# Kernel tuning notes

Measured on AMD Instinct MI355X. Metric: run time of the kernel, lower is better.

## Reference

```python
import jax, jax.numpy as jnp
import numpy as np

N, D, E = 200000, 256, 6400000
RATIO = 0.5
NEG_SLOPE = 0.2


def _xavier(key, shape, gain=1.414):
    fan_in, fan_out = shape[0], shape[1]
    limit = gain * (6.0 / (fan_in + fan_out)) ** 0.5
    return jax.random.uniform(key, shape, jnp.float32, -limit, limit)


def setup_inputs() -> dict:
    key = jax.random.key(0)
    ks = jax.random.split(key, 8)
    x = jax.random.normal(ks[0], (N, D), jnp.float32)
    edge_index = jax.random.randint(ks[1], (2, E), 0, N, dtype=jnp.int64)
    return {
        "x": x,
        "edge_index": edge_index,
        "w_s1": _xavier(ks[2], (2 * D, D)), "b_s1": jnp.zeros((D,), jnp.float32),
        "w_s2": _xavier(ks[3], (D, 1)),     "b_s2": jnp.zeros((1,), jnp.float32),
        "w_f1": _xavier(ks[4], (D, D // 2)), "b_f1": jnp.zeros((D // 2,), jnp.float32),
        "w_f2": _xavier(ks[5], (D // 2, 1)), "b_f2": jnp.zeros((1,), jnp.float32),
        "w_p": _xavier(ks[6], (D, D)),      "b_p": jnp.zeros((D,), jnp.float32),
        "alpha": jnp.float32(0.5), "beta": jnp.float32(0.5),
    }


def reference(x, edge_index, w_s1, b_s1, w_s2, b_s2, w_f1, b_f1, w_f2, b_f2, w_p, b_p, alpha, beta):
    num_nodes = x.shape[0]
    k = max(1, int(RATIO * num_nodes))
    lrelu = lambda v: jax.nn.leaky_relu(v, NEG_SLOPE)

    row, col = edge_index[0], edge_index[1]
    # degree(row, N): scatter-add of ones over source nodes
    deg = jax.ops.segment_sum(jnp.ones_like(row, dtype=x.dtype), row, num_segments=num_nodes)
    # F.normalize(p=2, dim=0) on the [N,1] degree column
    deg_norm = deg / jnp.maximum(jnp.sqrt(jnp.sum(deg * deg)), 1e-12)

    struct_in = jnp.concatenate([x, jnp.broadcast_to(deg_norm[:, None], x.shape)], axis=1)  # [N, 2D]
    struct_scores = (lrelu(struct_in @ w_s1 + b_s1) @ w_s2 + b_s2)[:, 0]  # dropout is eval no-op
    feat_scores = (lrelu(x @ w_f1 + b_f1) @ w_f2 + b_f2)[:, 0]

    a = jax.nn.sigmoid(alpha)
    b = jax.nn.sigmoid(beta)
    s = a + b
    scores = (a / s) * struct_scores + (b / s) * feat_scores  # [N]

    # single-graph top-k (batch=None default path)
    topk_scores, topk_idx = jax.lax.top_k(scores, k)
    x_pooled = lrelu(x[topk_idx] @ w_p + b_p)  # post_pool, dropout no-op

    # edge remap + compaction (valid edges first, -1 padding to keep static shape)
    node_map = jnp.full((num_nodes,), -1, dtype=jnp.int32).at[topk_idx].set(
        jnp.arange(k, dtype=jnp.int32))
    mr, mc = node_map[row], node_map[col]
    mask = (mr >= 0) & (mc >= 0)
    order = jnp.argsort(~mask, stable=True)  # stable: keeps original edge order among valid
    edge_index_pooled = jnp.stack([
        jnp.where(mask, mr, -1)[order],
        jnp.where(mask, mc, -1)[order],
    ])
    return x_pooled, edge_index_pooled, topk_scores
```

## Files before the change

### kernel.cpp

```cpp
#include <hip/hip_runtime.h>
#include <math.h>

typedef unsigned long long u64;
typedef unsigned int u32;
typedef unsigned short u16;
typedef __attribute__((ext_vector_type(8))) short bf16x8;
typedef __attribute__((ext_vector_type(4))) float f32x4;

#define D   256
#define ECH 16
#define EBLK (256*ECH)
#define BAND_W 4096
#define BAND_DELTA 1e-3f
#define HR  12544
#define HCH 32

__device__ __forceinline__ double lrelu(double v){ return v > 0.0 ? v : 0.2*v; }
__device__ __forceinline__ float  lreluf(float v){ return v > 0.0f ? v : 0.2f*v; }

__device__ __forceinline__ u16 f2bf(float f){
  union{float f; u32 u;} v; v.f = f;
  u32 r = v.u + 0x7FFFu + ((v.u >> 16) & 1u);
  return (u16)(r >> 16);
}
__device__ __forceinline__ float bf2f(u16 b){
  union{u32 u; float f;} v; v.u = ((u32)b) << 16; return v.f;
}

__global__ __launch_bounds__(256) void k_deghist(const int* __restrict__ row, int E,
                                                 u32* __restrict__ partial, int NR){
  __shared__ u32 h[HR];
  const int tid = threadIdx.x;
  const int r = blockIdx.x % NR;
  const int c = blockIdx.x / NR;
  for (int i = tid; i < HR; i += 256) h[i] = 0;
  __syncthreads();
  const int lo = r * HR;
  int CE = ((E + HCH - 1) / HCH + 3) & ~3;
  const int e0 = c * CE;
  const int e1 = min(e0 + CE, E);
  for (int e = e0 + tid*4; e < e1; e += 256*4){
    if (e + 3 < e1){
      int4 v = *(const int4*)(row + e);
      u32 d0 = (u32)(v.x - lo), d1 = (u32)(v.y - lo);
      u32 d2 = (u32)(v.z - lo), d3 = (u32)(v.w - lo);
      if (d0 < (u32)HR) atomicAdd(&h[d0], 1u);
      if (d1 < (u32)HR) atomicAdd(&h[d1], 1u);
      if (d2 < (u32)HR) atomicAdd(&h[d2], 1u);
      if (d3 < (u32)HR) atomicAdd(&h[d3], 1u);
    } else {
      for (int j = 0; j < 4 && e + j < e1; ++j){
        u32 d = (u32)(row[e+j] - lo);
        if (d < (u32)HR) atomicAdd(&h[d], 1u);
      }
    }
  }
  __syncthreads();
  u32* plane = partial + (size_t)blockIdx.x * HR;
  for (int i = tid; i < HR; i += 256) plane[i] = h[i];
}

__global__ void k_degred2(const u32* __restrict__ partial, int N, int NR,
                          int* __restrict__ deg, u64* __restrict__ out){
  __shared__ u64 sh[256];
  u64 local = 0;
  int stride = gridDim.x*blockDim.x;
  for (int i = blockIdx.x*blockDim.x + threadIdx.x; i < N; i += stride){
    int r = i / HR, off = i % HR;
    u32 s = 0;
    #pragma unroll 8
    for (int c = 0; c < HCH; ++c) s += partial[(size_t)(c*NR + r)*HR + off];
    deg[i] = (int)s;
    local += (u64)s * (u64)s;
  }
  sh[threadIdx.x] = local; __syncthreads();
  for (int s = 128; s > 0; s >>= 1){
    if (threadIdx.x < s) sh[threadIdx.x] += sh[threadIdx.x+s];
    __syncthreads();
  }
  if (threadIdx.x == 0) atomicAdd(out, sh[0]);
}

__global__ void k_prep(const float* __restrict__ wS1, const float* __restrict__ alpha,
                       const float* __restrict__ beta, const u64* __restrict__ sumsq,
                       double* __restrict__ s1b, double* __restrict__ scal,
                       float* __restrict__ s1bf, float* __restrict__ scalf){
  int j = threadIdx.x;
  double s = 0.0;
  for (int r = 0; r < D; ++r) s += (double)wS1[(D + r)*D + j];
  s1b[j] = s;
  s1bf[j] = (float)s;
  if (j == 0){
    double a = 1.0/(1.0 + exp(-(double)alpha[0]));
    double b = 1.0/(1.0 + exp(-(double)beta[0]));
    scal[0] = a/(a+b);
    scal[1] = b/(a+b);
    double dn = sqrt((double)(*sumsq));
    scal[2] = dn > 1e-12 ? dn : 1e-12;
    scalf[0] = (float)scal[0];
    scalf[1] = (float)scal[1];
    scalf[2] = (float)(1.0/scal[2]);
  }
}

__global__ void k_wsw(const float* __restrict__ wS1, const float* __restrict__ wF1,
                      u16* __restrict__ wswH, u16* __restrict__ wswL){
  int idx = blockIdx.x*blockDim.x + threadIdx.x;
  int i    = idx & 7;
  int lane = (idx >> 3) & 63;
  int sg   = (idx >> 9) & 7;
  int t    = idx >> 12;
  int k = sg*32 + ((lane >> 4) & 3)*8 + i;
  int c16 = lane & 15;
  float wv;
  if (t < 16) wv = wS1[k*256 + t*16 + c16];
  else        wv = wF1[k*128 + (t-16)*16 + c16];
  u16 h = f2bf(wv);
  float lo = wv - bf2f(h);
  wswH[idx] = h;
  wswL[idx] = f2bf(lo);
}

__global__ void k_wswP(const float* __restrict__ wP,
                       u16* __restrict__ wH, u16* __restrict__ wL){
  int idx = blockIdx.x*blockDim.x + threadIdx.x;
  int i    = idx & 7;
  int lane = (idx >> 3) & 63;
  int sg   = (idx >> 9) & 7;
  int t    = idx >> 12;
  int k = sg*32 + ((lane >> 4) & 3)*8 + i;
  float wv = wP[k*256 + t*16 + (lane & 15)];
  u16 h = f2bf(wv);
  float lo = wv - bf2f(h);
  wH[idx] = h;
  wL[idx] = f2bf(lo);
}

__global__ __launch_bounds__(512, 4) void k_scores_mfma(
    const float* __restrict__ x, const int* __restrict__ deg,
    const u16* __restrict__ wswH, const u16* __restrict__ wswL,
    const float* __restrict__ bS1, const float* __restrict__ wS2, const float* __restrict__ bS2,
    const float* __restrict__ bF1, const float* __restrict__ wF2, const float* __restrict__ bF2,
    const float* __restrict__ s1bf, const float* __restrict__ scalf,
    float* __restrict__ s32, u64* __restrict__ keys, int N)
{
  __shared__ u16 xsh[2][4096];
  __shared__ u16 xsl[2][4096];
  __shared__ float dnsh[64];
  __shared__ float part_s[64][9];
  __shared__ float part_f[64][9];

  const int tid  = threadIdx.x;
  const int lane = tid & 63;
  const int w    = tid >> 6;
  const int node0 = blockIdx.x * 64;

  if (tid < 64){
    int node = node0 + tid;
    dnsh[tid] = (node < N) ? ((float)deg[node] * scalf[2]) : 0.0f;
  }

  const int row_st = tid >> 3;
  const int seg_st = tid & 7;
  const int unit_w = row_st*8 + (seg_st ^ (row_st & 7));
  const float* srcbase = x + (size_t)(node0 + row_st)*D + seg_st*8;
  const bool rv = (node0 + row_st) < N;

  f32x4 acc[4][3];
  #pragma unroll
  for (int m = 0; m < 4; ++m)
    #pragma unroll
    for (int n = 0; n < 3; ++n) acc[m][n] = (f32x4){0.f,0.f,0.f,0.f};

  float xr[8];
  {
    if (rv){
      float4 a = *(const float4*)(srcbase);
      float4 b = *(const float4*)(srcbase + 4);
      xr[0]=a.x; xr[1]=a.y; xr[2]=a.z; xr[3]=a.w;
      xr[4]=b.x; xr[5]=b.y; xr[6]=b.z; xr[7]=b.w;
    } else {
      #pragma unroll
      for (int i = 0; i < 8; ++i) xr[i] = 0.f;
    }
  }

  #pragma unroll
  for (int c = 0; c < 4; ++c){
    const int pb = c & 1;
    {
      u16 h[8];
      #pragma unroll
      for (int i = 0; i < 8; ++i) h[i] = f2bf(xr[i]);
      uint4 H; H.x = (u32)h[0] | ((u32)h[1]<<16); H.y = (u32)h[2] | ((u32)h[3]<<16);
               H.z = (u32)h[4] | ((u32)h[5]<<16); H.w = (u32)h[6] | ((u32)h[7]<<16);
      u16 l[8];
      #pragma unroll
      for (int i = 0; i < 8; ++i) l[i] = f2bf(xr[i] - bf2f(h[i]));
      uint4 L; L.x = (u32)l[0] | ((u32)l[1]<<16); L.y = (u32)l[2] | ((u32)l[3]<<16);
               L.z = (u32)l[4] | ((u32)l[5]<<16); L.w = (u32)l[6] | ((u32)l[7]<<16);
      *(uint4*)&xsh[pb][unit_w*8] = H;
      *(uint4*)&xsl[pb][unit_w*8] = L;
    }
    if (c < 3){
      const float* sn = srcbase + (c+1)*64;
      if (rv){
        float4 a = *(const float4*)(sn);
        float4 b = *(const float4*)(sn + 4);
        xr[0]=a.x; xr[1]=a.y; xr[2]=a.z; xr[3]=a.w;
        xr[4]=b.x; xr[5]=b.y; xr[6]=b.z; xr[7]=b.w;
      }
    }
    __syncthreads();
    #pragma unroll
    for (int s = 0; s < 2; ++s){
      const int sg = c*2 + s;
      bf16x8 ah[4], al[4];
      #pragma unroll
      for (int mt = 0; mt < 4; ++mt){
        int row = mt*16 + (lane & 15);
        int seg = s*4 + (lane >> 4);
        int un  = row*8 + (seg ^ (row & 7));
        ah[mt] = *(const bf16x8*)&xsh[pb][un*8];
        al[mt] = *(const bf16x8*)&xsl[pb][un*8];
      }
      const int t0 = w*3;
      size_t o0 = ((size_t)(t0*8 + sg)*64 + lane)*8;
      bf16x8 bh = *(const bf16x8*)&wswH[o0];
      bf16x8 bl = *(const bf16x8*)&wswL[o0];
      #pragma unroll
      for (int nt = 0; nt < 3; ++nt){
        bf16x8 nbh = bh, nbl = bl;
        if (nt < 2){
          size_t on = ((size_t)((t0+nt+1)*8 + sg)*64 + lane)*8;
          nbh = *(const bf16x8*)&wswH[on];
          nbl = *(const bf16x8*)&wswL[on];
        }
        #pragma unroll
        for (int mt = 0; mt < 4; ++mt){
          acc[mt][nt] = __builtin_amdgcn_mfma_f32_16x16x32_bf16(ah[mt], bh, acc[mt][nt], 0,0,0);
          acc[mt][nt] = __builtin_amdgcn_mfma_f32_16x16x32_bf16(al[mt], bh, acc[mt][nt], 0,0,0);
          acc[mt][nt] = __builtin_amdgcn_mfma_f32_16x16x32_bf16(ah[mt], bl, acc[mt][nt], 0,0,0);
        }
        bh = nbh; bl = nbl;
      }
    }
    __syncthreads();
  }

  float dnl[4][4];
  #pragma unroll
  for (int mt = 0; mt < 4; ++mt)
    #pragma unroll
    for (int j = 0; j < 4; ++j)
      dnl[mt][j] = dnsh[mt*16 + (lane>>4)*4 + j];

  float ps[4][4], pf[4][4];
  #pragma unroll
  for (int mt = 0; mt < 4; ++mt)
    #pragma unroll
    for (int j = 0; j < 4; ++j){ ps[mt][j] = 0.f; pf[mt][j] = 0.f; }

  #pragma unroll
  for (int nt = 0; nt < 3; ++nt){
    const int t = w*3 + nt;
    const int c16 = lane & 15;
    const bool isS = (t < 16);
    const int col = isS ? t*16 + c16 : (t-16)*16 + c16;
    const float bias = isS ? bS1[col] : bF1[col];
    const float sbv  = isS ? s1bf[col] : 0.f;
    const float vv   = isS ? wS2[col] : wF2[col];
    #pragma unroll
    for (int mt = 0; mt < 4; ++mt){
      #pragma unroll
      for (int j = 0; j < 4; ++j){
        float v = acc[mt][nt][j] + bias + dnl[mt][j]*sbv;
        v = lreluf(v) * vv;
        v += __shfl_xor(v, 1);
        v += __shfl_xor(v, 2);
        v += __shfl_xor(v, 4);
        v += __shfl_xor(v, 8);
        if (isS) ps[mt][j] += v; else pf[mt][j] += v;
      }
    }
  }
  if ((lane & 15) == 0){
    #pragma unroll
    for (int mt = 0; mt < 4; ++mt)
      #pragma unroll
      for (int j = 0; j < 4; ++j){
        int row = mt*16 + (lane>>4)*4 + j;
        part_s[row][w] = ps[mt][j];
        part_f[row][w] = pf[mt][j];
      }
  }
  __syncthreads();
  if (tid < 64){
    int node = node0 + tid;
    if (node < N){
      float sv = 0.f, fv = 0.f;
      #pragma unroll
      for (int ww = 0; ww < 8; ++ww){ sv += part_s[tid][ww]; fv += part_f[tid][ww]; }
      float sc = scalf[0]*(sv + bS2[0]) + scalf[1]*(fv + bF2[0]);
      s32[node] = sc;
      u32 bits = __float_as_uint(sc);
      u32 ord = (bits >> 31) ? ~bits : (bits | 0x80000000u);
      keys[node] = ((u64)(~ord) << 32) | (u32)node;
    }
  }
}

__global__ void k_padkeys(u64* __restrict__ keys, int N, int SORTN){
  int i = N + blockIdx.x*blockDim.x + threadIdx.x;
  if (i < SORTN) keys[i] = ~0ULL;
}

__global__ __launch_bounds__(1024) void k_bsort_local8k(u64* __restrict__ keys){
  __shared__ u64 sk[8192];
  const int tid = threadIdx.x;
  const int base = blockIdx.x * 8192;
  #pragma unroll
  for (int e = 0; e < 8; ++e) sk[tid + e*1024] = keys[base + tid + e*1024];
  __syncthreads();
  for (int size = 2; size <= 8192; size <<= 1){
    for (int stride = size >> 1; stride > 0; stride >>= 1){
      #pragma unroll
      for (int pp = 0; pp < 4; ++pp){
        int p  = tid + pp*1024;
        int i  = 2*p - (p & (stride-1));
        int jj = i + stride;
        bool up = (((base + i) & size) == 0);
        u64 ki = sk[i], kj = sk[jj];
        if ((ki > kj) == up){ sk[i] = kj; sk[jj] = ki; }
      }
      __syncthreads();
    }
  }
  #pragma unroll
  for (int e = 0; e < 8; ++e) keys[base + tid + e*1024] = sk[tid + e*1024];
}

__global__ __launch_bounds__(1024) void k_bmerge_local8k(u64* __restrict__ keys, int size){
  __shared__ u64 sk[8192];
  const int tid = threadIdx.x;
  const int base = blockIdx.x * 8192;
  #pragma unroll
  for (int e = 0; e < 8; ++e) sk[tid + e*1024] = keys[base + tid + e*1024];
  __syncthreads();
  for (int stride = 4096; stride > 0; stride >>= 1){
    #pragma unroll
    for (int pp = 0; pp < 4; ++pp){
      int p  = tid + pp*1024;
      int i  = 2*p - (p & (stride-1));
      int jj = i + stride;
      bool up = (((base + i) & size) == 0);
      u64 ki = sk[i], kj = sk[jj];
      if ((ki > kj) == up){ sk[i] = kj; sk[jj] = ki; }
    }
    __syncthreads();
  }
  #pragma unroll
  for (int e = 0; e < 8; ++e) keys[base + tid + e*1024] = sk[tid + e*1024];
}

template<int NS>
__global__ void k_bpassM(u64* __restrict__ keys, int size, int stride){
  const int G = 1 << NS;
  u32 t = blockIdx.x*blockDim.x + threadIdx.x;
  u32 smin = (u32)stride >> (NS-1);
  u32 i0 = (t/smin)*(smin << NS) + (t % smin);
  u64 v[G];
  #pragma unroll
  for (int j = 0; j < G; ++j) v[j] = keys[i0 + (u32)j*smin];
  bool up = ((i0 & (u32)size) == 0);
  #pragma unroll
  for (int b = (G>>1); b >= 1; b >>= 1){
    #pragma unroll
    for (int j = 0; j < G; ++j){
      if ((j & b) == 0){
        u64 a = v[j], cc = v[j|b];
        if ((a > cc) == up){ v[j] = cc; v[j|b] = a; }
      }
    }
  }
  #pragma unroll
  for (int j = 0; j < G; ++j) keys[i0 + (u32)j*smin] = v[j];
}

__global__ void kr_cut(const u64* __restrict__ keys, int k, float* __restrict__ cutbuf,
                       int* __restrict__ r01){
  if (threadIdx.x == 0 && blockIdx.x == 0){
    u32 key32 = (u32)(keys[k-1] >> 32);
    u32 ord = ~key32;
    u32 u = (ord & 0x80000000u) ? (ord ^ 0x80000000u) : ~ord;
    float c = __uint_as_float(u);
    cutbuf[0] = c - BAND_DELTA;
    cutbuf[1] = c + BAND_DELTA;
    r01[0] = 0x7FFFFFFF;
    r01[1] = -1;
  }
}

__global__ __launch_bounds__(256) void kr_rescore(
    const u64* __restrict__ keys, const float* __restrict__ s32,
    const float* __restrict__ x, const int* __restrict__ deg,
    const float* __restrict__ wS1, const float* __restrict__ bS1,
    const float* __restrict__ wS2, const float* __restrict__ bS2,
    const float* __restrict__ wF1, const float* __restrict__ bF1,
    const float* __restrict__ wF2, const float* __restrict__ bF2,
    const double* __restrict__ s1b, const double* __restrict__ scal,
    const float* __restrict__ cutbuf, int* __restrict__ r01,
    double* __restrict__ bandS, int k, int N)
{
  const int r = k - BAND_W + blockIdx.x;
  if (r < 0 || r >= N) return;
  const int node = (int)(u32)(keys[r] & 0xFFFFFFFFULL);
  const float s = s32[node];
  if (s < cutbuf[0] || s > cutbuf[1]) return;

  const int tid = threadIdx.x;
  if (tid == 0){ atomicMin(&r01[0], r); atomicMax(&r01[1], r); }

  __shared__ float xr[256];
  __shared__ double rsp[4], rfp[4];
  xr[tid] = x[(size_t)node*D + tid];
  __syncthreads();

  const int j = tid;
  double accA = (double)bS1[j] + ((double)deg[node]/scal[2]) * s1b[j];
  double accB = (j < 128) ? (double)bF1[j] : 0.0;
  for (int rr = 0; rr < D; ++rr){
    double xv = (double)xr[rr];
    accA = fma(xv, (double)wS1[rr*D + j], accA);
    if (j < 128) accB = fma(xv, (double)wF1[rr*128 + j], accB);
  }
  double sp = lrelu(accA) * (double)wS2[j];
  double fp = (j < 128) ? lrelu(accB) * (double)wF2[j] : 0.0;

  const int lane = tid & 63, wave = tid >> 6;
  #pragma unroll
  for (int off = 32; off > 0; off >>= 1){
    sp += __shfl_down(sp, off);
    fp += __shfl_down(fp, off);
  }
  if (lane == 0){ rsp[wave] = sp; rfp[wave] = fp; }
  __syncthreads();
  if (tid == 0){
    double SP = rsp[0]+rsp[1]+rsp[2]+rsp[3];
    double FP = rfp[0]+rfp[1]+rfp[2]+rfp[3];
    bandS[blockIdx.x] = scal[0]*(SP + (double)bS2[0]) + scal[1]*(FP + (double)bF2[0]);
  }
}

__global__ __launch_bounds__(1024) void kr_bandsort(u64* __restrict__ keys,
    const double* __restrict__ bandS, const int* __restrict__ r01, int k){
  __shared__ double bs[8192];
  __shared__ int bi[8192];
  const int r0 = r01[0], r1 = r01[1];
  int nb = r1 - r0 + 1;
  if (nb <= 1) return;
  if (nb > 8192) nb = 8192;
  int M = 1; while (M < nb) M <<= 1;
  const int tid = threadIdx.x;
  const int sbase = r0 - (k - BAND_W);
  for (int m = tid; m < M; m += 1024){
    if (m < nb){ bs[m] = bandS[sbase + m]; bi[m] = (int)(u32)(keys[r0+m] & 0xFFFFFFFFULL); }
    else       { bs[m] = -1.0/0.0;         bi[m] = 0x7FFFFFFF; }
  }
  __syncthreads();
  for (int size = 2; size <= M; size <<= 1){
    for (int stride = size >> 1; stride > 0; stride >>= 1){
      for (int p = tid; p < (M >> 1); p += 1024){
        int i = 2*p - (p & (stride-1));
        int jj = i + stride;
        bool up = ((i & size) == 0);
        double si_ = bs[i], sj = bs[jj];
        int ii = bi[i], ij = bi[jj];
        bool gt = (si_ < sj) || (si_ == sj && ii > ij);
        if (gt == up){ bs[i]=sj; bs[jj]=si_; bi[i]=ij; bi[jj]=ii; }
      }
      __syncthreads();
    }
  }
  for (int m = tid; m < nb; m += 1024)
    keys[r0+m] = (u64)(u32)bi[m];
}

__global__ void k_finalize(const u64* __restrict__ keys, const float* __restrict__ s32,
                           int k, int* __restrict__ nmap, float* __restrict__ outS){
  int p = blockIdx.x*blockDim.x + threadIdx.x;
  if (p < k){
    int node = (int)(u32)(keys[p] & 0xFFFFFFFFULL);
    nmap[node] = p;
    outS[p] = s32[node];
  }
}

__global__ __launch_bounds__(512, 4) void k_xpool_mfma(
    const float* __restrict__ x, const u64* __restrict__ keys,
    const u16* __restrict__ wH, const u16* __restrict__ wL,
    const float* __restrict__ bP, float* __restrict__ out, int kk)
{
  __shared__ u16 xsh[2][4096];
  __shared__ u16 xsl[2][4096];

  const int tid  = threadIdx.x;
  const int lane = tid & 63;
  const int w    = tid >> 6;
  const int p0 = blockIdx.x * 64;
  if (p0 >= kk) return;

  const int row_st = tid >> 3;
  const int seg_st = tid & 7;
  const int unit_w = row_st*8 + (seg_st ^ (row_st & 7));
  int prow = p0 + row_st; if (prow >= kk) prow = kk - 1;
  const int node = (int)(u32)(keys[prow] & 0xFFFFFFFFULL);
  const float* srcbase = x + (size_t)node*D + seg_st*8;

  f32x4 acc[4][2];
  #pragma unroll
  for (int m = 0; m < 4; ++m){ acc[m][0] = (f32x4){0.f,0.f,0.f,0.f}; acc[m][1] = (f32x4){0.f,0.f,0.f,0.f}; }

  float xr[8];
  {
    float4 a = *(const float4*)(srcbase);
    float4 b = *(const float4*)(srcbase + 4);
    xr[0]=a.x; xr[1]=a.y; xr[2]=a.z; xr[3]=a.w;
    xr[4]=b.x; xr[5]=b.y; xr[6]=b.z; xr[7]=b.w;
  }

  #pragma unroll
  for (int c = 0; c < 4; ++c){
    const int pb = c & 1;
    {
      u16 h[8];
      #pragma unroll
      for (int i = 0; i < 8; ++i) h[i] = f2bf(xr[i]);
      uint4 H; H.x = (u32)h[0] | ((u32)h[1]<<16); H.y = (u32)h[2] | ((u32)h[3]<<16);
               H.z = (u32)h[4] | ((u32)h[5]<<16); H.w = (u32)h[6] | ((u32)h[7]<<16);
      u16 l[8];
      #pragma unroll
      for (int i = 0; i < 8; ++i) l[i] = f2bf(xr[i] - bf2f(h[i]));
      uint4 L; L.x = (u32)l[0] | ((u32)l[1]<<16); L.y = (u32)l[2] | ((u32)l[3]<<16);
               L.z = (u32)l[4] | ((u32)l[5]<<16); L.w = (u32)l[6] | ((u32)l[7]<<16);
      *(uint4*)&xsh[pb][unit_w*8] = H;
      *(uint4*)&xsl[pb][unit_w*8] = L;
    }
    if (c < 3){
      const float* sn = srcbase + (c+1)*64;
      float4 a = *(const float4*)(sn);
      float4 b = *(const float4*)(sn + 4);
      xr[0]=a.x; xr[1]=a.y; xr[2]=a.z; xr[3]=a.w;
      xr[4]=b.x; xr[5]=b.y; xr[6]=b.z; xr[7]=b.w;
    }
    __syncthreads();
    #pragma unroll
    for (int s = 0; s < 2; ++s){
      const int sg = c*2 + s;
      bf16x8 ah[4], al[4];
      #pragma unroll
      for (int mt = 0; mt < 4; ++mt){
        int row = mt*16 + (lane & 15);
        int seg = s*4 + (lane >> 4);
        int un  = row*8 + (seg ^ (row & 7));
        ah[mt] = *(const bf16x8*)&xsh[pb][un*8];
        al[mt] = *(const bf16x8*)&xsl[pb][un*8];
      }
      const int t0 = w*2;
      size_t o0 = ((size_t)(t0*8 + sg)*64 + lane)*8;
      bf16x8 bh = *(const bf16x8*)&wH[o0];
      bf16x8 bl = *(const bf16x8*)&wL[o0];
      #pragma unroll
      for (int nt = 0; nt < 2; ++nt){
        bf16x8 nbh = bh, nbl = bl;
        if (nt < 1){
          size_t on = ((size_t)((t0+1)*8 + sg)*64 + lane)*8;
          nbh = *(const bf16x8*)&wH[on];
          nbl = *(const bf16x8*)&wL[on];
        }
        #pragma unroll
        for (int mt = 0; mt < 4; ++mt){
          acc[mt][nt] = __builtin_amdgcn_mfma_f32_16x16x32_bf16(ah[mt], bh, acc[mt][nt], 0,0,0);
          acc[mt][nt] = __builtin_amdgcn_mfma_f32_16x16x32_bf16(al[mt], bh, acc[mt][nt], 0,0,0);
          acc[mt][nt] = __builtin_amdgcn_mfma_f32_16x16x32_bf16(ah[mt], bl, acc[mt][nt], 0,0,0);
        }
        bh = nbh; bl = nbl;
      }
    }
    __syncthreads();
  }

  const int c16 = lane & 15, r4 = (lane >> 4)*4;
  #pragma unroll
  for (int nt = 0; nt < 2; ++nt){
    const int col = (w*2 + nt)*16 + c16;
    const float bias = bP[col];
    #pragma unroll
    for (int mt = 0; mt < 4; ++mt){
      #pragma unroll
      for (int j = 0; j < 4; ++j){
        int p = p0 + mt*16 + r4 + j;
        if (p < kk) out[(size_t)p*D + col] = lreluf(acc[mt][nt][j] + bias);
      }
    }
  }
}

__global__ __launch_bounds__(256) void k_ecount(const int* __restrict__ erow, const int* __restrict__ ecol,
    const int* __restrict__ nmap, int E, int* __restrict__ bcount){
  __shared__ int sc[256];
  const int tid = threadIdx.x;
  const int base = blockIdx.x*EBLK + tid*ECH;
  int cnt = 0;
  #pragma unroll
  for (int q = 0; q < ECH; ++q){
    int e = base + q;
    if (e < E){
      if (nmap[erow[e]] >= 0 && nmap[ecol[e]] >= 0) cnt++;
    }
  }
  sc[tid] = cnt; __syncthreads();
  for (int s = 128; s > 0; s >>= 1){
    if (tid < s) sc[tid] += sc[tid+s];
    __syncthreads();
  }
  if (tid == 0) bcount[blockIdx.x] = sc[0];
}

__global__ __launch_bounds__(1024) void k_escan(const int* __restrict__ bcount, int nblk,
                                                int* __restrict__ boff, int* __restrict__ tot){
  __shared__ int sh[1024];
  const int tid = threadIdx.x;
  int carry = 0;
  for (int s = 0; s < nblk; s += 1024){
    int v = (s + tid < nblk) ? bcount[s+tid] : 0;
    sh[tid] = v; __syncthreads();
    for (int d = 1; d < 1024; d <<= 1){
      int t = (tid >= d) ? sh[tid-d] : 0;
      __syncthreads();
      sh[tid] += t;
      __syncthreads();
    }
    if (s + tid < nblk) boff[s+tid] = carry + sh[tid] - v;
    carry += sh[1023];
    __syncthreads();
  }
  if (tid == 0) *tot = carry;
}

__global__ void k_efill_tail(float* __restrict__ outR, float* __restrict__ outC,
                             const int* __restrict__ tot, int E){
  const int t0 = *tot;
  int stride = gridDim.x*blockDim.x;
  for (int i = t0 + blockIdx.x*blockDim.x + threadIdx.x; i < E; i += stride){
    outR[i] = -1.0f;
    outC[i] = -1.0f;
  }
}

__global__ __launch_bounds__(256) void k_escatter(const int* __restrict__ erow, const int* __restrict__ ecol,
    const int* __restrict__ nmap, int E, const int* __restrict__ boff,
    float* __restrict__ outR, float* __restrict__ outC){
  __shared__ int sc[256];
  const int tid = threadIdx.x;
  const int base = blockIdx.x*EBLK + tid*ECH;
  int mr[ECH], mc[ECH];
  int cnt = 0;
  #pragma unroll
  for (int q = 0; q < ECH; ++q){
    int e = base + q;
    int a = -1, b = -1;
    if (e < E){ a = nmap[erow[e]]; b = nmap[ecol[e]]; }
    mr[q] = a; mc[q] = b;
    if (a >= 0 && b >= 0) cnt++;
  }
  sc[tid] = cnt; __syncthreads();
  int v = cnt;
  for (int d = 1; d < 256; d <<= 1){
    int t = (tid >= d) ? sc[tid-d] : 0;
    __syncthreads();
    sc[tid] += t;
    __syncthreads();
  }
  int pos = boff[blockIdx.x] + sc[tid] - v;
  #pragma unroll
  for (int q = 0; q < ECH; ++q){
    if (mr[q] >= 0 && mc[q] >= 0){
      outR[pos] = (float)mr[q];
      outC[pos] = (float)mc[q];
      pos++;
    }
  }
}

extern "C" void kernel_launch(void* const* d_in, const int* in_sizes, int n_in,
                              void* d_out, int out_size, void* d_ws, size_t ws_size,
                              hipStream_t stream)
{
  const float* x   = (const float*)d_in[0];
  const int*   ei  = (const int*)d_in[1];
  const float* wS1 = (const float*)d_in[2];
  const float* bS1 = (const float*)d_in[3];
  const float* wS2 = (const float*)d_in[4];
  const float* bS2 = (const float*)d_in[5];
  const float* wF1 = (const float*)d_in[6];
  const float* bF1 = (const float*)d_in[7];
  const float* wF2 = (const float*)d_in[8];
  const float* bF2 = (const float*)d_in[9];
  const float* wP  = (const float*)d_in[10];
  const float* bP  = (const float*)d_in[11];
  const float* alpha = (const float*)d_in[12];
  const float* beta  = (const float*)d_in[13];
  (void)n_in; (void)out_size; (void)ws_size;

  const int N = in_sizes[0] / D;
  const int E = in_sizes[1] / 2;
  int k = (int)(0.5 * (double)N); if (k < 1) k = 1;
  int SORTN = 8192; while (SORTN < N) SORTN <<= 1;
  const int nblk_e = (E + EBLK - 1) / EBLK;
  const int NR = (N + HR - 1) / HR;

  char* w = (char*)d_ws;
  size_t off = 0;
  auto alloc = [&](size_t bytes)->char*{
    char* p = w + off;
    off = (off + bytes + 255) & ~(size_t)255;
    return p;
  };
  float*  s32    = (float*) alloc((size_t)N*4);
  u64*    keys   = (u64*)   alloc((size_t)SORTN*8);
  int*    deg    = (int*)   alloc((size_t)N*4);
  int*    nmap   = (int*)   alloc((size_t)N*4);
  double* s1b    = (double*)alloc((size_t)D*8);
  float*  s1bf   = (float*) alloc((size_t)D*4);
  double* scal   = (double*)alloc(4*8);
  float*  scalf  = (float*) alloc(4*4);
  u64*    sumsq  = (u64*)   alloc(8);
  float*  cutbuf = (float*) alloc(2*4);
  int*    r01    = (int*)   alloc(2*4);
  int*    tot    = (int*)   alloc(4);
  double* bandS  = (double*)alloc((size_t)2*BAND_W*8);
  u16*    wswH   = (u16*)   alloc((size_t)98304*2);
  u16*    wswL   = (u16*)   alloc((size_t)98304*2);
  u16*    wswPH  = (u16*)   alloc((size_t)65536*2);
  u16*    wswPL  = (u16*)   alloc((size_t)65536*2);
  int*    bcount = (int*)   alloc((size_t)nblk_e*4);
  int*    boff   = (int*)   alloc((size_t)nblk_e*4);

  float* outX  = (float*)d_out;
  float* outER = outX  + (size_t)k*D;
  float* outEC = outER + (size_t)E;
  float* outS  = outEC + (size_t)E;

  u32* partial = (u32*)outER;

  hipMemsetAsync(sumsq, 0,    8,           stream);
  hipMemsetAsync(nmap,  0xFF, (size_t)N*4, stream);

  k_deghist<<<NR*HCH, 256, 0, stream>>>(ei, E, partial, NR);
  k_degred2<<<1024, 256, 0, stream>>>(partial, N, NR, deg, sumsq);
  k_prep   <<<1,    D,   0, stream>>>(wS1, alpha, beta, sumsq, s1b, scal, s1bf, scalf);
  k_wsw    <<<384,  256, 0, stream>>>(wS1, wF1, wswH, wswL);
  k_wswP   <<<256,  256, 0, stream>>>(wP, wswPH, wswPL);
  k_scores_mfma<<<(N + 63)/64, 512, 0, stream>>>(x, deg, wswH, wswL,
                                                 bS1, wS2, bS2, bF1, wF2, bF2,
                                                 s1bf, scalf, s32, keys, N);
  k_padkeys<<<(SORTN - N + 255)/256, 256, 0, stream>>>(keys, N, SORTN);

  k_bsort_local8k<<<SORTN/8192, 1024, 0, stream>>>(keys);
  for (int size = 16384; size <= SORTN; size <<= 1){
    int stride = size >> 1;
    while (stride >= 8192){
      int ns = 1;
      while (ns < 4 && (stride >> ns) >= 8192) ns++;
      switch (ns){
        case 1: k_bpassM<1><<<SORTN/2/256,  256, 0, stream>>>(keys, size, stride); break;
        case 2: k_bpassM<2><<<SORTN/4/256,  256, 0, stream>>>(keys, size, stride); break;
        case 3: k_bpassM<3><<<SORTN/8/256,  256, 0, stream>>>(keys, size, stride); break;
        default:k_bpassM<4><<<SORTN/16/256, 256, 0, stream>>>(keys, size, stride); break;
      }
      stride >>= ns;
    }
    k_bmerge_local8k<<<SORTN/8192, 1024, 0, stream>>>(keys, size);
  }

  kr_cut     <<<1, 64, 0, stream>>>(keys, k, cutbuf, r01);
  kr_rescore <<<2*BAND_W, 256, 0, stream>>>(keys, s32, x, deg, wS1,bS1,wS2,bS2,
                                            wF1,bF1,wF2,bF2, s1b, scal,
                                            cutbuf, r01, bandS, k, N);
  kr_bandsort<<<1, 1024, 0, stream>>>(keys, bandS, r01, k);

  k_finalize<<<(k+255)/256, 256, 0, stream>>>(keys, s32, k, nmap, outS);
  k_xpool_mfma<<<(k+63)/64, 512, 0, stream>>>(x, keys, wswPH, wswPL, bP, outX, k);
  k_ecount  <<<nblk_e, 256, 0, stream>>>(ei, ei+E, nmap, E, bcount);
  k_escan   <<<1, 1024, 0, stream>>>(bcount, nblk_e, boff, tot);
  k_efill_tail<<<1024, 256, 0, stream>>>(outER, outEC, tot, E);
  k_escatter<<<nblk_e, 256, 0, stream>>>(ei, ei+E, nmap, E, boff, outER, outEC);
}
```

Before: 828.8 us.

## Drop weight low-part MFMA terms, pack degree histogram in 16-bit bins, fuse key padding

```diff
diff --git a/kernel.cpp b/kernel.cpp
--- a/kernel.cpp
+++ b/kernel.cpp
@@ -11,8 +11,8 @@
 #define ECH 16
 #define EBLK (256*ECH)
 #define BAND_W 4096
-#define BAND_DELTA 1e-3f
-#define HR  12544
+#define BAND_DELTA 2e-2f
+#define HR  25088
 #define HCH 32
 
 __device__ __forceinline__ double lrelu(double v){ return v > 0.0 ? v : 0.2*v; }
@@ -29,11 +29,11 @@
 
 __global__ __launch_bounds__(256) void k_deghist(const int* __restrict__ row, int E,
                                                  u32* __restrict__ partial, int NR){
-  __shared__ u32 h[HR];
+  __shared__ u32 h[HR/2];
   const int tid = threadIdx.x;
   const int r = blockIdx.x % NR;
   const int c = blockIdx.x / NR;
-  for (int i = tid; i < HR; i += 256) h[i] = 0;
+  for (int i = tid; i < HR/2; i += 256) h[i] = 0;
   __syncthreads();
   const int lo = r * HR;
   int CE = ((E + HCH - 1) / HCH + 3) & ~3;
@@ -44,20 +44,20 @@
       int4 v = *(const int4*)(row + e);
       u32 d0 = (u32)(v.x - lo), d1 = (u32)(v.y - lo);
       u32 d2 = (u32)(v.z - lo), d3 = (u32)(v.w - lo);
-      if (d0 < (u32)HR) atomicAdd(&h[d0], 1u);
-      if (d1 < (u32)HR) atomicAdd(&h[d1], 1u);
-      if (d2 < (u32)HR) atomicAdd(&h[d2], 1u);
-      if (d3 < (u32)HR) atomicAdd(&h[d3], 1u);
+      if (d0 < (u32)HR) atomicAdd(&h[d0 >> 1], 1u << ((d0 & 1)*16));
+      if (d1 < (u32)HR) atomicAdd(&h[d1 >> 1], 1u << ((d1 & 1)*16));
+      if (d2 < (u32)HR) atomicAdd(&h[d2 >> 1], 1u << ((d2 & 1)*16));
+      if (d3 < (u32)HR) atomicAdd(&h[d3 >> 1], 1u << ((d3 & 1)*16));
     } else {
       for (int j = 0; j < 4 && e + j < e1; ++j){
         u32 d = (u32)(row[e+j] - lo);
-        if (d < (u32)HR) atomicAdd(&h[d], 1u);
+        if (d < (u32)HR) atomicAdd(&h[d >> 1], 1u << ((d & 1)*16));
       }
     }
   }
   __syncthreads();
-  u32* plane = partial + (size_t)blockIdx.x * HR;
-  for (int i = tid; i < HR; i += 256) plane[i] = h[i];
+  u32* plane = partial + (size_t)blockIdx.x * (HR/2);
+  for (int i = tid; i < HR/2; i += 256) plane[i] = h[i];
 }
 
 __global__ void k_degred2(const u32* __restrict__ partial, int N, int NR,
@@ -67,9 +67,11 @@
   int stride = gridDim.x*blockDim.x;
   for (int i = blockIdx.x*blockDim.x + threadIdx.x; i < N; i += stride){
     int r = i / HR, off = i % HR;
+    const int word = off >> 1, shift = (off & 1)*16;
     u32 s = 0;
     #pragma unroll 8
-    for (int c = 0; c < HCH; ++c) s += partial[(size_t)(c*NR + r)*HR + off];
+    for (int c = 0; c < HCH; ++c)
+      s += (partial[(size_t)(c*NR + r)*(HR/2) + word] >> shift) & 0xFFFFu;
     deg[i] = (int)s;
     local += (u64)s * (u64)s;
   }
@@ -104,7 +106,7 @@
 }
 
 __global__ void k_wsw(const float* __restrict__ wS1, const float* __restrict__ wF1,
-                      u16* __restrict__ wswH, u16* __restrict__ wswL){
+                      u16* __restrict__ wswH){
   int idx = blockIdx.x*blockDim.x + threadIdx.x;
   int i    = idx & 7;
   int lane = (idx >> 3) & 63;
@@ -115,34 +117,26 @@
   float wv;
   if (t < 16) wv = wS1[k*256 + t*16 + c16];
   else        wv = wF1[k*128 + (t-16)*16 + c16];
-  u16 h = f2bf(wv);
-  float lo = wv - bf2f(h);
-  wswH[idx] = h;
-  wswL[idx] = f2bf(lo);
-}
-
-__global__ void k_wswP(const float* __restrict__ wP,
-                       u16* __restrict__ wH, u16* __restrict__ wL){
+  wswH[idx] = f2bf(wv);
+}
+
+__global__ void k_wswP(const float* __restrict__ wP, u16* __restrict__ wH){
   int idx = blockIdx.x*blockDim.x + threadIdx.x;
   int i    = idx & 7;
   int lane = (idx >> 3) & 63;
   int sg   = (idx >> 9) & 7;
   int t    = idx >> 12;
   int k = sg*32 + ((lane >> 4) & 3)*8 + i;
-  float wv = wP[k*256 + t*16 + (lane & 15)];
-  u16 h = f2bf(wv);
-  float lo = wv - bf2f(h);
-  wH[idx] = h;
-  wL[idx] = f2bf(lo);
+  wH[idx] = f2bf(wP[k*256 + t*16 + (lane & 15)]);
 }
 
 __global__ __launch_bounds__(512, 4) void k_scores_mfma(
     const float* __restrict__ x, const int* __restrict__ deg,
-    const u16* __restrict__ wswH, const u16* __restrict__ wswL,
+    const u16* __restrict__ wswH,
     const float* __restrict__ bS1, const float* __restrict__ wS2, const float* __restrict__ bS2,
     const float* __restrict__ bF1, const float* __restrict__ wF2, const float* __restrict__ bF2,
     const float* __restrict__ s1bf, const float* __restrict__ scalf,
-    float* __restrict__ s32, u64* __restrict__ keys, int N)
+    float* __restrict__ s32, u64* __restrict__ keys, int N, int SORTN)
 {
   __shared__ u16 xsh[2][4096];
   __shared__ u16 xsl[2][4096];
@@ -154,6 +148,14 @@
   const int lane = tid & 63;
   const int w    = tid >> 6;
   const int node0 = blockIdx.x * 64;
+
+  if (node0 >= N){
+    if (tid < 64){
+      int i = node0 + tid;
+      if (i < SORTN) keys[i] = ~0ULL;
+    }
+    return;
+  }
 
   if (tid < 64){
     int node = node0 + tid;
@@ -227,22 +229,19 @@
       const int t0 = w*3;
       size_t o0 = ((size_t)(t0*8 + sg)*64 + lane)*8;
       bf16x8 bh = *(const bf16x8*)&wswH[o0];
-      bf16x8 bl = *(const bf16x8*)&wswL[o0];
       #pragma unroll
       for (int nt = 0; nt < 3; ++nt){
-        bf16x8 nbh = bh, nbl = bl;
+        bf16x8 nbh = bh;
         if (nt < 2){
           size_t on = ((size_t)((t0+nt+1)*8 + sg)*64 + lane)*8;
           nbh = *(const bf16x8*)&wswH[on];
-          nbl = *(const bf16x8*)&wswL[on];
         }
         #pragma unroll
         for (int mt = 0; mt < 4; ++mt){
           acc[mt][nt] = __builtin_amdgcn_mfma_f32_16x16x32_bf16(ah[mt], bh, acc[mt][nt], 0,0,0);
           acc[mt][nt] = __builtin_amdgcn_mfma_f32_16x16x32_bf16(al[mt], bh, acc[mt][nt], 0,0,0);
-          acc[mt][nt] = __builtin_amdgcn_mfma_f32_16x16x32_bf16(ah[mt], bl, acc[mt][nt], 0,0,0);
         }
-        bh = nbh; bl = nbl;
+        bh = nbh;
       }
     }
     __syncthreads();
@@ -306,13 +305,11 @@
       u32 bits = __float_as_uint(sc);
       u32 ord = (bits >> 31) ? ~bits : (bits | 0x80000000u);
       keys[node] = ((u64)(~ord) << 32) | (u32)node;
-    }
-  }
-}
-
-__global__ void k_padkeys(u64* __restrict__ keys, int N, int SORTN){
-  int i = N + blockIdx.x*blockDim.x + threadIdx.x;
-  if (i < SORTN) keys[i] = ~0ULL;
+    } else {
+      int i = node0 + tid;
+      if (i < SORTN) keys[i] = ~0ULL;
+    }
+  }
 }
 
 __global__ __launch_bounds__(1024) void k_bsort_local8k(u64* __restrict__ keys){
@@ -498,7 +495,7 @@
 
 __global__ __launch_bounds__(512, 4) void k_xpool_mfma(
     const float* __restrict__ x, const u64* __restrict__ keys,
-    const u16* __restrict__ wH, const u16* __restrict__ wL,
+    const u16* __restrict__ wH,
     const float* __restrict__ bP, float* __restrict__ out, int kk)
 {
   __shared__ u16 xsh[2][4096];
@@ -569,22 +566,19 @@
       const int t0 = w*2;
       size_t o0 = ((size_t)(t0*8 + sg)*64 + lane)*8;
       bf16x8 bh = *(const bf16x8*)&wH[o0];
-      bf16x8 bl = *(const bf16x8*)&wL[o0];
       #pragma unroll
       for (int nt = 0; nt < 2; ++nt){
-        bf16x8 nbh = bh, nbl = bl;
+        bf16x8 nbh = bh;
         if (nt < 1){
           size_t on = ((size_t)((t0+1)*8 + sg)*64 + lane)*8;
           nbh = *(const bf16x8*)&wH[on];
-          nbl = *(const bf16x8*)&wL[on];
         }
         #pragma unroll
         for (int mt = 0; mt < 4; ++mt){
           acc[mt][nt] = __builtin_amdgcn_mfma_f32_16x16x32_bf16(ah[mt], bh, acc[mt][nt], 0,0,0);
           acc[mt][nt] = __builtin_amdgcn_mfma_f32_16x16x32_bf16(al[mt], bh, acc[mt][nt], 0,0,0);
-          acc[mt][nt] = __builtin_amdgcn_mfma_f32_16x16x32_bf16(ah[mt], bl, acc[mt][nt], 0,0,0);
         }
-        bh = nbh; bl = nbl;
+        bh = nbh;
       }
     }
     __syncthreads();
@@ -741,9 +735,7 @@
   int*    tot    = (int*)   alloc(4);
   double* bandS  = (double*)alloc((size_t)2*BAND_W*8);
   u16*    wswH   = (u16*)   alloc((size_t)98304*2);
-  u16*    wswL   = (u16*)   alloc((size_t)98304*2);
   u16*    wswPH  = (u16*)   alloc((size_t)65536*2);
-  u16*    wswPL  = (u16*)   alloc((size_t)65536*2);
   int*    bcount = (int*)   alloc((size_t)nblk_e*4);
   int*    boff   = (int*)   alloc((size_t)nblk_e*4);
 
@@ -760,12 +752,11 @@
   k_deghist<<<NR*HCH, 256, 0, stream>>>(ei, E, partial, NR);
   k_degred2<<<1024, 256, 0, stream>>>(partial, N, NR, deg, sumsq);
   k_prep   <<<1,    D,   0, stream>>>(wS1, alpha, beta, sumsq, s1b, scal, s1bf, scalf);
-  k_wsw    <<<384,  256, 0, stream>>>(wS1, wF1, wswH, wswL);
-  k_wswP   <<<256,  256, 0, stream>>>(wP, wswPH, wswPL);
-  k_scores_mfma<<<(N + 63)/64, 512, 0, stream>>>(x, deg, wswH, wswL,
-                                                 bS1, wS2, bS2, bF1, wF2, bF2,
-                                                 s1bf, scalf, s32, keys, N);
-  k_padkeys<<<(SORTN - N + 255)/256, 256, 0, stream>>>(keys, N, SORTN);
+  k_wsw    <<<384,  256, 0, stream>>>(wS1, wF1, wswH);
+  k_wswP   <<<256,  256, 0, stream>>>(wP, wswPH);
+  k_scores_mfma<<<SORTN/64, 512, 0, stream>>>(x, deg, wswH,
+                                              bS1, wS2, bS2, bF1, wF2, bF2,
+                                              s1bf, scalf, s32, keys, N, SORTN);
 
   k_bsort_local8k<<<SORTN/8192, 1024, 0, stream>>>(keys);
   for (int size = 16384; size <= SORTN; size <<= 1){
@@ -791,7 +782,7 @@
   kr_bandsort<<<1, 1024, 0, stream>>>(keys, bandS, r01, k);
 
   k_finalize<<<(k+255)/256, 256, 0, stream>>>(keys, s32, k, nmap, outS);
-  k_xpool_mfma<<<(k+63)/64, 512, 0, stream>>>(x, keys, wswPH, wswPL, bP, outX, k);
+  k_xpool_mfma<<<(k+63)/64, 512, 0, stream>>>(x, keys, wswPH, bP, outX, k);
   k_ecount  <<<nblk_e, 256, 0, stream>>>(ei, ei+E, nmap, E, bcount);
   k_escan   <<<1, 1024, 0, stream>>>(bcount, nblk_e, boff, tot);
   k_efill_tail<<<1024, 256, 0, stream>>>(outER, outEC, tot, E);
```

Result: slower. 933.5 us (+12.6%).

## Pack degree histogram into 16-bit bins, fold key padding, unroll band rescoring

Applied to the files above, without the earlier changes.

```diff
diff --git a/kernel.cpp b/kernel.cpp
--- a/kernel.cpp
+++ b/kernel.cpp
@@ -12,7 +12,7 @@
 #define EBLK (256*ECH)
 #define BAND_W 4096
 #define BAND_DELTA 1e-3f
-#define HR  12544
+#define HR  25088
 #define HCH 32
 
 __device__ __forceinline__ double lrelu(double v){ return v > 0.0 ? v : 0.2*v; }
@@ -29,11 +29,11 @@
 
 __global__ __launch_bounds__(256) void k_deghist(const int* __restrict__ row, int E,
                                                  u32* __restrict__ partial, int NR){
-  __shared__ u32 h[HR];
+  __shared__ u32 h[HR/2];
   const int tid = threadIdx.x;
   const int r = blockIdx.x % NR;
   const int c = blockIdx.x / NR;
-  for (int i = tid; i < HR; i += 256) h[i] = 0;
+  for (int i = tid; i < HR/2; i += 256) h[i] = 0;
   __syncthreads();
   const int lo = r * HR;
   int CE = ((E + HCH - 1) / HCH + 3) & ~3;
@@ -44,20 +44,20 @@
       int4 v = *(const int4*)(row + e);
       u32 d0 = (u32)(v.x - lo), d1 = (u32)(v.y - lo);
       u32 d2 = (u32)(v.z - lo), d3 = (u32)(v.w - lo);
-      if (d0 < (u32)HR) atomicAdd(&h[d0], 1u);
-      if (d1 < (u32)HR) atomicAdd(&h[d1], 1u);
-      if (d2 < (u32)HR) atomicAdd(&h[d2], 1u);
-      if (d3 < (u32)HR) atomicAdd(&h[d3], 1u);
+      if (d0 < (u32)HR) atomicAdd(&h[d0 >> 1], 1u << ((d0 & 1)*16));
+      if (d1 < (u32)HR) atomicAdd(&h[d1 >> 1], 1u << ((d1 & 1)*16));
+      if (d2 < (u32)HR) atomicAdd(&h[d2 >> 1], 1u << ((d2 & 1)*16));
+      if (d3 < (u32)HR) atomicAdd(&h[d3 >> 1], 1u << ((d3 & 1)*16));
     } else {
       for (int j = 0; j < 4 && e + j < e1; ++j){
         u32 d = (u32)(row[e+j] - lo);
-        if (d < (u32)HR) atomicAdd(&h[d], 1u);
+        if (d < (u32)HR) atomicAdd(&h[d >> 1], 1u << ((d & 1)*16));
       }
     }
   }
   __syncthreads();
-  u32* plane = partial + (size_t)blockIdx.x * HR;
-  for (int i = tid; i < HR; i += 256) plane[i] = h[i];
+  u32* plane = partial + (size_t)blockIdx.x * (HR/2);
+  for (int i = tid; i < HR/2; i += 256) plane[i] = h[i];
 }
 
 __global__ void k_degred2(const u32* __restrict__ partial, int N, int NR,
@@ -67,9 +67,11 @@
   int stride = gridDim.x*blockDim.x;
   for (int i = blockIdx.x*blockDim.x + threadIdx.x; i < N; i += stride){
     int r = i / HR, off = i % HR;
+    const int word = off >> 1, shift = (off & 1)*16;
     u32 s = 0;
     #pragma unroll 8
-    for (int c = 0; c < HCH; ++c) s += partial[(size_t)(c*NR + r)*HR + off];
+    for (int c = 0; c < HCH; ++c)
+      s += (partial[(size_t)(c*NR + r)*(HR/2) + word] >> shift) & 0xFFFFu;
     deg[i] = (int)s;
     local += (u64)s * (u64)s;
   }
@@ -142,7 +144,7 @@
     const float* __restrict__ bS1, const float* __restrict__ wS2, const float* __restrict__ bS2,
     const float* __restrict__ bF1, const float* __restrict__ wF2, const float* __restrict__ bF2,
     const float* __restrict__ s1bf, const float* __restrict__ scalf,
-    float* __restrict__ s32, u64* __restrict__ keys, int N)
+    float* __restrict__ s32, u64* __restrict__ keys, int N, int SORTN)
 {
   __shared__ u16 xsh[2][4096];
   __shared__ u16 xsl[2][4096];
@@ -154,6 +156,14 @@
   const int lane = tid & 63;
   const int w    = tid >> 6;
   const int node0 = blockIdx.x * 64;
+
+  if (node0 >= N){
+    if (tid < 64){
+      int i = node0 + tid;
+      if (i < SORTN) keys[i] = ~0ULL;
+    }
+    return;
+  }
 
   if (tid < 64){
     int node = node0 + tid;
@@ -306,13 +316,11 @@
       u32 bits = __float_as_uint(sc);
       u32 ord = (bits >> 31) ? ~bits : (bits | 0x80000000u);
       keys[node] = ((u64)(~ord) << 32) | (u32)node;
-    }
-  }
-}
-
-__global__ void k_padkeys(u64* __restrict__ keys, int N, int SORTN){
-  int i = N + blockIdx.x*blockDim.x + threadIdx.x;
-  if (i < SORTN) keys[i] = ~0ULL;
+    } else {
+      int i = node0 + tid;
+      if (i < SORTN) keys[i] = ~0ULL;
+    }
+  }
 }
 
 __global__ __launch_bounds__(1024) void k_bsort_local8k(u64* __restrict__ keys){
@@ -427,15 +435,38 @@
   __syncthreads();
 
   const int j = tid;
-  double accA = (double)bS1[j] + ((double)deg[node]/scal[2]) * s1b[j];
-  double accB = (j < 128) ? (double)bF1[j] : 0.0;
-  for (int rr = 0; rr < D; ++rr){
-    double xv = (double)xr[rr];
-    accA = fma(xv, (double)wS1[rr*D + j], accA);
-    if (j < 128) accB = fma(xv, (double)wF1[rr*128 + j], accB);
-  }
+  double a0=0.0, a1=0.0, a2=0.0, a3=0.0;
+  double b0=0.0, b1=0.0, b2=0.0, b3=0.0;
+  if (j < 128){
+    for (int rr = 0; rr < D; rr += 4){
+      double x0 = (double)xr[rr+0], x1 = (double)xr[rr+1];
+      double x2 = (double)xr[rr+2], x3 = (double)xr[rr+3];
+      a0 = fma(x0, (double)wS1[(rr+0)*D + j], a0);
+      a1 = fma(x1, (double)wS1[(rr+1)*D + j], a1);
+      a2 = fma(x2, (double)wS1[(rr+2)*D + j], a2);
+      a3 = fma(x3, (double)wS1[(rr+3)*D + j], a3);
+      b0 = fma(x0, (double)wF1[(rr+0)*128 + j], b0);
+      b1 = fma(x1, (double)wF1[(rr+1)*128 + j], b1);
+      b2 = fma(x2, (double)wF1[(rr+2)*128 + j], b2);
+      b3 = fma(x3, (double)wF1[(rr+3)*128 + j], b3);
+    }
+  } else {
+    for (int rr = 0; rr < D; rr += 4){
+      double x0 = (double)xr[rr+0], x1 = (double)xr[rr+1];
+      double x2 = (double)xr[rr+2], x3 = (double)xr[rr+3];
+      a0 = fma(x0, (double)wS1[(rr+0)*D + j], a0);
+      a1 = fma(x1, (double)wS1[(rr+1)*D + j], a1);
+      a2 = fma(x2, (double)wS1[(rr+2)*D + j], a2);
+      a3 = fma(x3, (double)wS1[(rr+3)*D + j], a3);
+    }
+  }
+  double accA = ((a0+a1)+(a2+a3)) + (double)bS1[j] + ((double)deg[node]/scal[2]) * s1b[j];
   double sp = lrelu(accA) * (double)wS2[j];
-  double fp = (j < 128) ? lrelu(accB) * (double)wF2[j] : 0.0;
+  double fp = 0.0;
+  if (j < 128){
+    double accB = ((b0+b1)+(b2+b3)) + (double)bF1[j];
+    fp = lrelu(accB) * (double)wF2[j];
+  }
 
   const int lane = tid & 63, wave = tid >> 6;
   #pragma unroll
@@ -762,10 +793,9 @@
   k_prep   <<<1,    D,   0, stream>>>(wS1, alpha, beta, sumsq, s1b, scal, s1bf, scalf);
   k_wsw    <<<384,  256, 0, stream>>>(wS1, wF1, wswH, wswL);
   k_wswP   <<<256,  256, 0, stream>>>(wP, wswPH, wswPL);
-  k_scores_mfma<<<(N + 63)/64, 512, 0, stream>>>(x, deg, wswH, wswL,
-                                                 bS1, wS2, bS2, bF1, wF2, bF2,
-                                                 s1bf, scalf, s32, keys, N);
-  k_padkeys<<<(SORTN - N + 255)/256, 256, 0, stream>>>(keys, N, SORTN);
+  k_scores_mfma<<<SORTN/64, 512, 0, stream>>>(x, deg, wswH, wswL,
+                                              bS1, wS2, bS2, bF1, wF2, bF2,
+                                              s1bf, scalf, s32, keys, N, SORTN);
 
   k_bsort_local8k<<<SORTN/8192, 1024, 0, stream>>>(keys);
   for (int size = 16384; size <= SORTN; size <<= 1){
```

After: 766.5 us. 7.5% less time.
